# Kernel tuning notes

Hardware: AMD Instinct MI355X
Metric: run time of the kernel (lower is better)

Reference implementation:

```python
import jax, jax.numpy as jnp
import numpy as np


def _conv3x3(x, w, b):
    # NCHW conv, stride 1, pad 1
    y = jax.lax.conv_general_dilated(x, w, (1, 1), ((1, 1), (1, 1)),
                                     dimension_numbers=('NCHW', 'OIHW', 'NCHW'))
    return y + b[None, :, None, None]


def _deform_conv3x3(x, offset, w):
    # Deformable conv v1: 3x3, stride 1, pad 1, 1 deformable group, no bias.
    # offset: [B, 18, H, W] laid out as (dy_k, dx_k) for k = 0..8 (row-major taps).
    B, C, H, W = x.shape
    K = 9
    off = offset.reshape(B, K, 2, H, W)
    ky, kx = jnp.meshgrid(jnp.arange(3), jnp.arange(3), indexing='ij')
    ky = (ky.reshape(K) - 1).astype(x.dtype)  # kernel tap y-offset, pad=1
    kx = (kx.reshape(K) - 1).astype(x.dtype)
    hh = jnp.arange(H, dtype=x.dtype)
    ww = jnp.arange(W, dtype=x.dtype)
    # sampling locations [B, K, H, W]
    sy = hh[None, None, :, None] + ky[None, :, None, None] + off[:, :, 0]
    sx = ww[None, None, None, :] + kx[None, :, None, None] + off[:, :, 1]
    y0 = jnp.floor(sy)
    x0 = jnp.floor(sx)
    ly = sy - y0  # fractional parts
    lx = sx - x0
    x_flat = x.reshape(B, C, H * W)

    def gather(yi, xi, wgt):
        # zero-padding semantics: corners outside the image contribute 0
        valid = (yi >= 0) & (yi < H) & (xi >= 0) & (xi < W)
        idx = (jnp.clip(yi, 0, H - 1).astype(jnp.int32) * W
               + jnp.clip(xi, 0, W - 1).astype(jnp.int32)).reshape(B, 1, K * H * W)
        v = jnp.take_along_axis(x_flat, idx, axis=2).reshape(B, C, K, H, W)
        return v * (wgt * valid.astype(x.dtype))[:, None]

    sampled = (gather(y0,     x0,     (1 - ly) * (1 - lx))
             + gather(y0,     x0 + 1, (1 - ly) * lx)
             + gather(y0 + 1, x0,     ly * (1 - lx))
             + gather(y0 + 1, x0 + 1, ly * lx))  # [B, C, K, H, W]
    return jnp.einsum('bckhw,ock->bohw', sampled, w.reshape(w.shape[0], C, K))


def setup_inputs() -> dict:
    key = jax.random.key(0)
    ks = jax.random.split(key, 8)
    C, O = 256, 256
    return {
        'kernel': jax.random.normal(ks[0], (16, C, 16, 16), jnp.float32),
        'search': jax.random.normal(ks[1], (16, C, 32, 32), jnp.float32),
        'Toffset_w': jax.random.normal(ks[2], (18, C, 3, 3), jnp.float32) * 0.02,
        'Toffset_b': jnp.zeros((18,), jnp.float32),
        'Tdeform_w': jax.random.normal(ks[3], (O, C, 3, 3), jnp.float32) * 0.02,
        'Soffset_w': jax.random.normal(ks[4], (18, C, 3, 3), jnp.float32) * 0.02,
        'Soffset_b': jnp.zeros((18,), jnp.float32),
        'Sdeform_w': jax.random.normal(ks[5], (O, C, 3, 3), jnp.float32) * 0.02,
    }


def reference(kernel, search, Toffset_w, Toffset_b, Tdeform_w,
              Soffset_w, Soffset_b, Sdeform_w):
    kernel_offset = _conv3x3(kernel, Toffset_w, Toffset_b)
    kernel_out = _deform_conv3x3(kernel, kernel_offset, Tdeform_w)
    search_offset = _conv3x3(search, Soffset_w, Soffset_b)
    search_out = _deform_conv3x3(search, search_offset, Sdeform_w)
    return (kernel_out, search_out, kernel_offset, search_offset)
```

## Files before the change

### kernel.cpp

```cpp
#include <hip/hip_runtime.h>

#define CIN   256
#define OC    256
#define K_TOT 2304
#define CCH   32
#define NCHK  8
#define KCH   288
#define SSTR  296
#define DM    64

#define N_DW  (OC * K_TOT)
#define N_OW  (32 * K_TOT)
#define N_CVT (2 * N_DW + 2 * N_OW)
#define CVT_BLOCKS (N_CVT / 4 / 512)
#define XT_K_ELEMS ((size_t)16 * 256 * 256)
#define XT_S_ELEMS ((size_t)16 * 1024 * 256)

typedef short  bf16x8 __attribute__((ext_vector_type(8)));
typedef float  f32x4  __attribute__((ext_vector_type(4)));
typedef unsigned short ushort_t;

__device__ __forceinline__ ushort_t f2bf(float f) {
    unsigned u = __builtin_bit_cast(unsigned, f);
    u += 0x7fffu + ((u >> 16) & 1u);
    return (ushort_t)(u >> 16);
}
__device__ __forceinline__ float bf2f(short s) {
    return __builtin_bit_cast(float, ((unsigned)(unsigned short)s) << 16);
}

__global__ __launch_bounds__(512) void prep_k(
    const float* __restrict__ tdw, const float* __restrict__ sdw,
    const float* __restrict__ tow, const float* __restrict__ sow,
    const float* __restrict__ kin, const float* __restrict__ sin_,
    ushort_t* __restrict__ wk_d, ushort_t* __restrict__ ws_d,
    ushort_t* __restrict__ wk_o, ushort_t* __restrict__ ws_o,
    ushort_t* __restrict__ xt_k, ushort_t* __restrict__ xt_s)
{
    __shared__ ushort_t tile[64][264];

    if (blockIdx.x == 0 && threadIdx.x < 64) {
        ushort4 z = {0, 0, 0, 0};
        *(ushort4*)&xt_s[XT_S_ELEMS + (size_t)threadIdx.x * 4] = z;
    }

    if (blockIdx.x < CVT_BLOCKS) {
        const int i = (blockIdx.x * 512 + threadIdx.x) * 4;
        const float* src; ushort_t* dst; int j; bool offw = false;
        if (i < N_DW)                    { src = tdw; dst = wk_d; j = i; }
        else if (i < 2 * N_DW)           { src = sdw; dst = ws_d; j = i - N_DW; }
        else if (i < 2 * N_DW + N_OW)    { src = tow; dst = wk_o; j = i - 2 * N_DW; offw = true; }
        else                             { src = sow; dst = ws_o; j = i - 2 * N_DW - N_OW; offw = true; }
        const int oc = j / K_TOT;
        const int k  = j - oc * K_TOT;
        const int cc = k / KCH;
        const int r  = k - cc * KCH;
        const int tap = r >> 5;
        const int cl  = r & 31;
        ushort4 o4 = {0, 0, 0, 0};
        if (!offw || oc < 18) {
            const float* sp = &src[((size_t)oc * CIN + cc * 32 + cl) * 9 + tap];
            o4.x = f2bf(sp[0]); o4.y = f2bf(sp[9]); o4.z = f2bf(sp[18]); o4.w = f2bf(sp[27]);
        }
        *(ushort4*)&dst[j] = o4;
        return;
    }

    const int bx2 = blockIdx.x - CVT_BLOCKS;
    int H, W, b, px0; const float* x; ushort_t* xt;
    if (bx2 < 64) {
        H = 16; W = 16; x = kin; xt = xt_k;
        b = bx2 >> 2; px0 = (bx2 & 3) * 64;
    } else {
        int t2 = bx2 - 64;
        H = 32; W = 32; x = sin_; xt = xt_s;
        b = t2 >> 4; px0 = (t2 & 15) * 64;
    }
    const int HW = H * W;
    const int t = threadIdx.x, lane = t & 63, wv = t >> 6;
    const float* xb = x + (size_t)b * CIN * HW;

    for (int it = 0; it < 8; ++it) {
        const int ch = wv * 32 + it * 4 + (lane >> 4);
        const int pq = (lane & 15) * 4;
        float4 v = *(const float4*)&xb[(size_t)ch * HW + px0 + pq];
        tile[pq + 0][ch] = f2bf(v.x);
        tile[pq + 1][ch] = f2bf(v.y);
        tile[pq + 2][ch] = f2bf(v.z);
        tile[pq + 3][ch] = f2bf(v.w);
    }
    __syncthreads();
    for (int it = 0; it < 4; ++it) {
        const int px = it * 16 + wv * 2 + (lane >> 5);
        const int cg = (lane & 31) * 8;
        bf16x8 v = *(const bf16x8*)&tile[px][cg];
        *(bf16x8*)&xt[((size_t)b * HW + px0 + px) * 256 + cg] = v;
    }
}

__device__ __forceinline__ void dcn_load4(
    bf16x8* c, const ushort_t* __restrict__ xtb, int4 id, int cb)
{
    c[0] = *(const bf16x8*)&xtb[(size_t)id.x * 256 + cb];
    c[1] = *(const bf16x8*)&xtb[(size_t)id.y * 256 + cb];
    c[2] = *(const bf16x8*)&xtb[(size_t)id.z * 256 + cb];
    c[3] = *(const bf16x8*)&xtb[(size_t)id.w * 256 + cb];
}
__device__ __forceinline__ void dcn_proc2(
    ushort_t* swb, int so, const bf16x8* c, float4 wt)
{
    bf16x8 r;
#pragma unroll
    for (int j = 0; j < 8; ++j) {
        const float v = wt.x * bf2f(c[0][j]) + wt.y * bf2f(c[1][j])
                      + wt.z * bf2f(c[2][j]) + wt.w * bf2f(c[3][j]);
        r[j] = (short)f2bf(v);
    }
    *(bf16x8*)&swb[so] = r;
}

__global__ __launch_bounds__(512, 4) void deform_gemm_k(
    const ushort_t* __restrict__ xt_k,
    const ushort_t* __restrict__ kwo, const float* __restrict__ kbias,
    float* __restrict__ koff, const ushort_t* __restrict__ kwd,
    float* __restrict__ kout,
    const ushort_t* __restrict__ xt_s,
    const ushort_t* __restrict__ swo, const float* __restrict__ sbias,
    float* __restrict__ soff, const ushort_t* __restrict__ swd,
    float* __restrict__ sout)
{
    __shared__ __align__(16) char  uni[64512];
    __shared__ __align__(16) float offsL[18][64];

    float    (*sred)[64][36] = (float(*)[64][36])uni;
    ushort_t (*smp)[SSTR]    = (ushort_t(*)[SSTR])uni;
    int      (*sidx)[9][4]   = (int(*)[9][4])(uni + 37888);
    float    (*swt)[9][4]    = (float(*)[9][4])(uni + 47104);

    int H, W, sh, b, px0; int zrel;
    const ushort_t *xt, *wgo, *wgd; const float* bias; float *ooff, *out;
    if (blockIdx.x < 64) {
        const int xcd = blockIdx.x & 7, i = blockIdx.x >> 3;
        H = 16; W = 16; sh = 4; xt = xt_k; wgo = kwo; bias = kbias;
        ooff = koff; wgd = kwd; out = kout;
        b = xcd + 8 * (i & 1); px0 = (i >> 1) * 64;
        zrel = (int)(XT_K_ELEMS + XT_S_ELEMS - (size_t)b * 256 * 256);
    } else {
        const int t2 = blockIdx.x - 64;
        const int xcd = t2 & 7, i = t2 >> 3;
        H = 32; W = 32; sh = 5; xt = xt_s; wgo = swo; bias = sbias;
        ooff = soff; wgd = swd; out = sout;
        b = xcd + 8 * (i & 1); px0 = (i >> 1) * 64;
        zrel = (int)(XT_S_ELEMS - (size_t)b * 1024 * 256);
    }
    const int HW = H * W;
    const int t = threadIdx.x, lane = t & 63, wv = t >> 6;
    const int l15 = lane & 15;
    const int cg8 = (lane >> 4) * 8;
    const ushort_t* xtb = xt + (size_t)b * HW * 256;

    {
        const int kh = wv;
        int h[4], wc[4];
#pragma unroll
        for (int mt = 0; mt < 4; ++mt) {
            const int px = px0 + mt * 16 + l15;
            h[mt]  = px >> sh;
            wc[mt] = px & (W - 1);
        }
        const ushort_t* wrow0 = wgo + (size_t)(l15)      * K_TOT + cg8;
        const ushort_t* wrow1 = wgo + (size_t)(16 + l15) * K_TOT + cg8;
        const int cb = kh * 32 + cg8;
        const size_t kg0 = (size_t)kh * KCH;

        f32x4 acc[4][2] = {};
#pragma unroll
        for (int ks = 0; ks < 9; ++ks) {
            const bf16x8 b0 = *(const bf16x8*)&wrow0[kg0 + (size_t)ks * 32];
            const bf16x8 b1 = *(const bf16x8*)&wrow1[kg0 + (size_t)ks * 32];
            const int dy = ks / 3 - 1, dx = ks % 3 - 1;
            bf16x8 a[4];
#pragma unroll
            for (int mt = 0; mt < 4; ++mt) {
                const int y  = h[mt] + dy;
                const int xx = wc[mt] + dx;
                const bool ok = ((unsigned)y < (unsigned)H) && ((unsigned)xx < (unsigned)W);
                const int off = ok ? (((y << sh) + xx) * 256 + cb) : (zrel + cb);
                a[mt] = *(const bf16x8*)&xtb[off];
            }
#pragma unroll
            for (int mt = 0; mt < 4; ++mt) {
                acc[mt][0] = __builtin_amdgcn_mfma_f32_16x16x32_bf16(a[mt], b0, acc[mt][0], 0, 0, 0);
                acc[mt][1] = __builtin_amdgcn_mfma_f32_16x16x32_bf16(a[mt], b1, acc[mt][1], 0, 0, 0);
            }
        }

        if (kh > 0) {
#pragma unroll
            for (int mt = 0; mt < 4; ++mt)
#pragma unroll
                for (int nt = 0; nt < 2; ++nt)
                    *(float4*)&sred[kh - 1][lane][(mt * 2 + nt) * 4] = *(float4*)&acc[mt][nt];
        }
        __syncthreads();
        if (kh == 0) {
            const int prow = (lane >> 4) * 4;
#pragma unroll
            for (int nt = 0; nt < 2; ++nt) {
                const int oc = nt * 16 + l15;
                if (oc < 18) {
                    const float bs = bias[oc];
#pragma unroll
                    for (int mt = 0; mt < 4; ++mt) {
                        float4 r = *(float4*)&acc[mt][nt];
#pragma unroll
                        for (int q = 0; q < 7; ++q) {
                            const float4 o = *(const float4*)&sred[q][lane][(mt * 2 + nt) * 4];
                            r.x += o.x; r.y += o.y; r.z += o.z; r.w += o.w;
                        }
                        r.x += bs; r.y += bs; r.z += bs; r.w += bs;
                        *(float4*)(ooff + ((size_t)b * 18 + oc) * HW + px0 + mt * 16 + prow) = r;
                        *(float4*)&offsL[oc][mt * 16 + prow] = r;
                    }
                }
            }
        }
        __syncthreads();
    }

#pragma unroll
    for (int u = 0; u < 2; ++u) {
        const int s = t + u * 512;
        if (s < DM * 9) {
            const int p = s / 9, k = s - 9 * p;
            const int pix = px0 + p;
            const int hh = pix >> sh;
            const int ww = pix & (W - 1);
            const float dy = offsL[2 * k    ][p];
            const float dx = offsL[2 * k + 1][p];
            const float sy = (float)(hh + k / 3 - 1) + dy;
            const float sx = (float)(ww + k % 3 - 1) + dx;
            const float y0f = floorf(sy), x0f = floorf(sx);
            const float ly = sy - y0f, lx = sx - x0f;
            const int y0 = (int)y0f, x0 = (int)x0f;
#pragma unroll
            for (int j = 0; j < 4; ++j) {
                const int yy = y0 + (j >> 1);
                const int xx = x0 + (j & 1);
                const bool ok = ((unsigned)yy < (unsigned)H) && ((unsigned)xx < (unsigned)W);
                sidx[p][k][j] = min(max(yy, 0), H - 1) * W + min(max(xx, 0), W - 1);
                const float wj = ((j >> 1) ? ly : 1.f - ly) * ((j & 1) ? lx : 1.f - lx);
                swt[p][k][j] = ok ? wj : 0.f;
            }
        }
    }
    __syncthreads();

    const int ocb = wv * 32;
    const bool live4 = (t < 256);

    const int g0  = t >> 2;
    const int cgE = (t & 3) * 8;
    int uso[5];
#pragma unroll
    for (int q = 0; q < 5; ++q) {
        const int g  = g0 + q * 128;
        const int px = g / 9, tap = g - 9 * px;
        uso[q] = px * SSTR + tap * 32 + (t & 3) * 8;
    }

    const ushort_t* wrow0 = wgd + (size_t)(ocb      + l15) * K_TOT + cg8;
    const ushort_t* wrow1 = wgd + (size_t)(ocb + 16 + l15) * K_TOT + cg8;
    ushort_t* smpb = &smp[0][0];
    const int4*   sidxF = (const int4*)  &sidx[0][0][0];
    const float4* swtF  = (const float4*)&swt [0][0][0];

    f32x4 acc[4][2] = {};

    for (int cc = 0; cc < NCHK; ++cc) {
        const int cb = cc * 32 + cgE;
        const size_t kg0 = (size_t)cc * KCH;

        bf16x8 cA[4], cB[4];
        float4 wA, wB;
        bf16x8 bq[2][2];
        { const int4 id = sidxF[g0];       wA = swtF[g0];       dcn_load4(cA, xtb, id, cb); }
        { const int4 id = sidxF[g0 + 128]; wB = swtF[g0 + 128]; dcn_load4(cB, xtb, id, cb); }
        bq[0][0] = *(const bf16x8*)&wrow0[kg0];
        bq[0][1] = *(const bf16x8*)&wrow1[kg0];

        dcn_proc2(smpb, uso[0], cA, wA);
        { const int4 id = sidxF[g0 + 256]; wA = swtF[g0 + 256]; dcn_load4(cA, xtb, id, cb); }
        dcn_proc2(smpb, uso[1], cB, wB);
        { const int4 id = sidxF[g0 + 384]; wB = swtF[g0 + 384]; dcn_load4(cB, xtb, id, cb); }
        dcn_proc2(smpb, uso[2], cA, wA);
        if (live4) { const int4 id = sidxF[g0 + 512]; wA = swtF[g0 + 512]; dcn_load4(cA, xtb, id, cb); }
        dcn_proc2(smpb, uso[3], cB, wB);
        if (live4) dcn_proc2(smpb, uso[4], cA, wA);

        asm volatile("s_waitcnt lgkmcnt(0)" ::: "memory");
        __builtin_amdgcn_sched_barrier(0);
        __builtin_amdgcn_s_barrier();
        __builtin_amdgcn_sched_barrier(0);

        __builtin_amdgcn_s_setprio(1);
#pragma unroll
        for (int ks = 0; ks < 9; ++ks) {
            if (ks < 8) {
                bq[(ks + 1) & 1][0] = *(const bf16x8*)&wrow0[kg0 + (size_t)(ks + 1) * 32];
                bq[(ks + 1) & 1][1] = *(const bf16x8*)&wrow1[kg0 + (size_t)(ks + 1) * 32];
            }
            bf16x8 a[4];
#pragma unroll
            for (int mt = 0; mt < 4; ++mt)
                a[mt] = *(const bf16x8*)&smp[mt * 16 + l15][ks * 32 + cg8];
#pragma unroll
            for (int mt = 0; mt < 4; ++mt) {
                acc[mt][0] = __builtin_amdgcn_mfma_f32_16x16x32_bf16(a[mt], bq[ks & 1][0], acc[mt][0], 0, 0, 0);
                acc[mt][1] = __builtin_amdgcn_mfma_f32_16x16x32_bf16(a[mt], bq[ks & 1][1], acc[mt][1], 0, 0, 0);
            }
        }
        __builtin_amdgcn_s_setprio(0);

        if (cc < NCHK - 1) {
            __builtin_amdgcn_sched_barrier(0);
            __builtin_amdgcn_s_barrier();
            __builtin_amdgcn_sched_barrier(0);
        }
    }

    const int prow = (lane >> 4) * 4;
#pragma unroll
    for (int mt = 0; mt < 4; ++mt) {
#pragma unroll
        for (int nt = 0; nt < 2; ++nt) {
            const int oc = ocb + nt * 16 + l15;
            float* op = out + ((size_t)b * OC + oc) * HW + px0 + mt * 16 + prow;
            *(float4*)op = *(float4*)&acc[mt][nt];
        }
    }
}

extern "C" void kernel_launch(void* const* d_in, const int* in_sizes, int n_in,
                              void* d_out, int out_size, void* d_ws, size_t ws_size,
                              hipStream_t stream) {
    const float* kin = (const float*)d_in[0];
    const float* sin_ = (const float*)d_in[1];
    const float* tow = (const float*)d_in[2];
    const float* tob = (const float*)d_in[3];
    const float* tdw = (const float*)d_in[4];
    const float* sow = (const float*)d_in[5];
    const float* sob = (const float*)d_in[6];
    const float* sdw = (const float*)d_in[7];

    float* out = (float*)d_out;
    float* out_k  = out;
    float* out_s  = out_k + (size_t)16 * 256 * 16 * 16;
    float* out_ko = out_s + (size_t)16 * 256 * 32 * 32;
    float* out_so = out_ko + (size_t)16 * 18 * 16 * 16;

    ushort_t* wk_d = (ushort_t*)d_ws;
    ushort_t* ws_d = wk_d + N_DW;
    ushort_t* wk_o = ws_d + N_DW;
    ushort_t* ws_o = wk_o + N_OW;
    ushort_t* xt_k = ws_o + N_OW;
    ushort_t* xt_s = xt_k + XT_K_ELEMS;

    prep_k<<<dim3(CVT_BLOCKS + 320), 512, 0, stream>>>(
        tdw, sdw, tow, sow, kin, sin_,
        wk_d, ws_d, wk_o, ws_o, xt_k, xt_s);

    deform_gemm_k<<<dim3(320), 512, 0, stream>>>(
        xt_k, wk_o, tob, out_ko, wk_d, out_k,
        xt_s, ws_o, sob, out_so, ws_d, out_s);
}
```

Measured before the change: 201.1 us.

## Shrink LDS footprint with tree reduction and fp16/int16 sampling tables

Replaces the 8-way split-K offset-conv reduction, which staged seven partial tiles in shared memory, with a 3-level tree reduction that needs only four staging slots. Sampling indices are stored as int16 and bilinear weights as fp16, halving their shared-memory tables. Together this cuts shared memory from about 64.5KB to 47KB, and the launch bound is raised to 6 waves per SIMD so more blocks can be resident per CU. In exchange it adds extra barriers to the reduction and loses some precision in the bilinear weights, which are now fp16 instead of fp32.

Result: slower. 235.9 us (+17.3%).

```diff
diff --git a/kernel.cpp b/kernel.cpp
--- a/kernel.cpp
+++ b/kernel.cpp
@@ -18,6 +18,8 @@
 
 typedef short  bf16x8 __attribute__((ext_vector_type(8)));
 typedef float  f32x4  __attribute__((ext_vector_type(4)));
+typedef short  sh4    __attribute__((ext_vector_type(4)));
+typedef _Float16 h4   __attribute__((ext_vector_type(4)));
 typedef unsigned short ushort_t;
 
 __device__ __forceinline__ ushort_t f2bf(float f) {
@@ -119,7 +121,7 @@
     *(bf16x8*)&swb[so] = r;
 }
 
-__global__ __launch_bounds__(512, 4) void deform_gemm_k(
+__global__ __launch_bounds__(512, 6) void deform_gemm_k(
     const ushort_t* __restrict__ xt_k,
     const ushort_t* __restrict__ kwo, const float* __restrict__ kbias,
     float* __restrict__ koff, const ushort_t* __restrict__ kwd,
@@ -129,13 +131,13 @@
     float* __restrict__ soff, const ushort_t* __restrict__ swd,
     float* __restrict__ sout)
 {
-    __shared__ __align__(16) char  uni[64512];
+    __shared__ __align__(16) char  uni[47104];
     __shared__ __align__(16) float offsL[18][64];
 
-    float    (*sred)[64][36] = (float(*)[64][36])uni;
-    ushort_t (*smp)[SSTR]    = (ushort_t(*)[SSTR])uni;
-    int      (*sidx)[9][4]   = (int(*)[9][4])(uni + 37888);
-    float    (*swt)[9][4]    = (float(*)[9][4])(uni + 47104);
+    float    (*red)[64][36] = (float(*)[64][36])uni;
+    ushort_t (*smp)[SSTR]   = (ushort_t(*)[SSTR])uni;
+    short    (*sidxS)[9][4] = (short(*)[9][4])(uni + 37888);
+    _Float16 (*swtH)[9][4]  = (_Float16(*)[9][4])(uni + 42496);
 
     int H, W, sh, b, px0; int zrel;
     const ushort_t *xt, *wgo, *wgd; const float* bias; float *ooff, *out;
@@ -195,12 +197,50 @@
             }
         }
 
-        if (kh > 0) {
+        if (kh >= 4) {
 #pragma unroll
             for (int mt = 0; mt < 4; ++mt)
 #pragma unroll
                 for (int nt = 0; nt < 2; ++nt)
-                    *(float4*)&sred[kh - 1][lane][(mt * 2 + nt) * 4] = *(float4*)&acc[mt][nt];
+                    *(float4*)&red[kh - 4][lane][(mt * 2 + nt) * 4] = *(float4*)&acc[mt][nt];
+        }
+        __syncthreads();
+        if (kh < 4) {
+#pragma unroll
+            for (int mt = 0; mt < 4; ++mt)
+#pragma unroll
+                for (int nt = 0; nt < 2; ++nt) {
+                    const float4 o = *(const float4*)&red[kh][lane][(mt * 2 + nt) * 4];
+                    acc[mt][nt].x += o.x; acc[mt][nt].y += o.y;
+                    acc[mt][nt].z += o.z; acc[mt][nt].w += o.w;
+                }
+        }
+        __syncthreads();
+        if (kh == 2 || kh == 3) {
+#pragma unroll
+            for (int mt = 0; mt < 4; ++mt)
+#pragma unroll
+                for (int nt = 0; nt < 2; ++nt)
+                    *(float4*)&red[kh - 2][lane][(mt * 2 + nt) * 4] = *(float4*)&acc[mt][nt];
+        }
+        __syncthreads();
+        if (kh < 2) {
+#pragma unroll
+            for (int mt = 0; mt < 4; ++mt)
+#pragma unroll
+                for (int nt = 0; nt < 2; ++nt) {
+                    const float4 o = *(const float4*)&red[kh][lane][(mt * 2 + nt) * 4];
+                    acc[mt][nt].x += o.x; acc[mt][nt].y += o.y;
+                    acc[mt][nt].z += o.z; acc[mt][nt].w += o.w;
+                }
+        }
+        __syncthreads();
+        if (kh == 1) {
+#pragma unroll
+            for (int mt = 0; mt < 4; ++mt)
+#pragma unroll
+                for (int nt = 0; nt < 2; ++nt)
+                    *(float4*)&red[0][lane][(mt * 2 + nt) * 4] = *(float4*)&acc[mt][nt];
         }
         __syncthreads();
         if (kh == 0) {
@@ -213,12 +253,9 @@
 #pragma unroll
                     for (int mt = 0; mt < 4; ++mt) {
                         float4 r = *(float4*)&acc[mt][nt];
-#pragma unroll
-                        for (int q = 0; q < 7; ++q) {
-                            const float4 o = *(const float4*)&sred[q][lane][(mt * 2 + nt) * 4];
-                            r.x += o.x; r.y += o.y; r.z += o.z; r.w += o.w;
-                        }
-                        r.x += bs; r.y += bs; r.z += bs; r.w += bs;
+                        const float4 o = *(const float4*)&red[0][lane][(mt * 2 + nt) * 4];
+                        r.x += o.x + bs; r.y += o.y + bs;
+                        r.z += o.z + bs; r.w += o.w + bs;
                         *(float4*)(ooff + ((size_t)b * 18 + oc) * HW + px0 + mt * 16 + prow) = r;
                         *(float4*)&offsL[oc][mt * 16 + prow] = r;
                     }
@@ -248,9 +285,9 @@
                 const int yy = y0 + (j >> 1);
                 const int xx = x0 + (j & 1);
                 const bool ok = ((unsigned)yy < (unsigned)H) && ((unsigned)xx < (unsigned)W);
-                sidx[p][k][j] = min(max(yy, 0), H - 1) * W + min(max(xx, 0), W - 1);
+                sidxS[p][k][j] = (short)(min(max(yy, 0), H - 1) * W + min(max(xx, 0), W - 1));
                 const float wj = ((j >> 1) ? ly : 1.f - ly) * ((j & 1) ? lx : 1.f - lx);
-                swt[p][k][j] = ok ? wj : 0.f;
+                swtH[p][k][j] = (_Float16)(ok ? wj : 0.f);
             }
         }
     }
@@ -272,8 +309,8 @@
     const ushort_t* wrow0 = wgd + (size_t)(ocb      + l15) * K_TOT + cg8;
     const ushort_t* wrow1 = wgd + (size_t)(ocb + 16 + l15) * K_TOT + cg8;
     ushort_t* smpb = &smp[0][0];
-    const int4*   sidxF = (const int4*)  &sidx[0][0][0];
-    const float4* swtF  = (const float4*)&swt [0][0][0];
+    const sh4* sidxF = (const sh4*)(uni + 37888);
+    const h4*  swtF  = (const h4*) (uni + 42496);
 
     f32x4 acc[4][2] = {};
 
@@ -284,17 +321,42 @@
         bf16x8 cA[4], cB[4];
         float4 wA, wB;
         bf16x8 bq[2][2];
-        { const int4 id = sidxF[g0];       wA = swtF[g0];       dcn_load4(cA, xtb, id, cb); }
-        { const int4 id = sidxF[g0 + 128]; wB = swtF[g0 + 128]; dcn_load4(cB, xtb, id, cb); }
+        {
+            const sh4 iv = sidxF[g0]; const h4 wvv = swtF[g0];
+            const int4 id = {iv.x, iv.y, iv.z, iv.w};
+            wA = (float4){(float)wvv.x, (float)wvv.y, (float)wvv.z, (float)wvv.w};
+            dcn_load4(cA, xtb, id, cb);
+        }
+        {
+            const sh4 iv = sidxF[g0 + 128]; const h4 wvv = swtF[g0 + 128];
+            const int4 id = {iv.x, iv.y, iv.z, iv.w};
+            wB = (float4){(float)wvv.x, (float)wvv.y, (float)wvv.z, (float)wvv.w};
+            dcn_load4(cB, xtb, id, cb);
+        }
         bq[0][0] = *(const bf16x8*)&wrow0[kg0];
         bq[0][1] = *(const bf16x8*)&wrow1[kg0];
 
         dcn_proc2(smpb, uso[0], cA, wA);
-        { const int4 id = sidxF[g0 + 256]; wA = swtF[g0 + 256]; dcn_load4(cA, xtb, id, cb); }
+        {
+            const sh4 iv = sidxF[g0 + 256]; const h4 wvv = swtF[g0 + 256];
+            const int4 id = {iv.x, iv.y, iv.z, iv.w};
+            wA = (float4){(float)wvv.x, (float)wvv.y, (float)wvv.z, (float)wvv.w};
+            dcn_load4(cA, xtb, id, cb);
+        }
         dcn_proc2(smpb, uso[1], cB, wB);
-        { const int4 id = sidxF[g0 + 384]; wB = swtF[g0 + 384]; dcn_load4(cB, xtb, id, cb); }
+        {
+            const sh4 iv = sidxF[g0 + 384]; const h4 wvv = swtF[g0 + 384];
+            const int4 id = {iv.x, iv.y, iv.z, iv.w};
+            wB = (float4){(float)wvv.x, (float)wvv.y, (float)wvv.z, (float)wvv.w};
+            dcn_load4(cB, xtb, id, cb);
+        }
         dcn_proc2(smpb, uso[2], cA, wA);
-        if (live4) { const int4 id = sidxF[g0 + 512]; wA = swtF[g0 + 512]; dcn_load4(cA, xtb, id, cb); }
+        if (live4) {
+            const sh4 iv = sidxF[g0 + 512]; const h4 wvv = swtF[g0 + 512];
+            const int4 id = {iv.x, iv.y, iv.z, iv.w};
+            wA = (float4){(float)wvv.x, (float)wvv.y, (float)wvv.z, (float)wvv.w};
+            dcn_load4(cA, xtb, id, cb);
+        }
         dcn_proc2(smpb, uso[3], cB, wB);
         if (live4) dcn_proc2(smpb, uso[4], cA, wA);
 
```
